# Kernel optimization log

Hardware: AMD Instinct MI355X
Metric: run time of the kernel (lower is better)

The kernel has to match this reference:

```python
import jax, jax.numpy as jnp
import numpy as np


def setup_inputs() -> dict:
    key = jax.random.key(0)
    k1, k2, k3 = jax.random.split(key, 3)
    B, L, C, H, W = 64, 64, 256, 8, 8
    z = jax.random.normal(k1, (B, L, C, H, W), dtype=jnp.float32)
    # KalmanFilter learned params: gain projection and state-transition (1x1 channel maps)
    W_gain = jax.random.normal(k2, (C, C), dtype=jnp.float32) * (1.0 / np.sqrt(C))
    b_gain = jnp.zeros((C,), dtype=jnp.float32)
    W_pred = jax.random.normal(k3, (C, C), dtype=jnp.float32) * (1.0 / np.sqrt(C))
    b_pred = jnp.zeros((C,), dtype=jnp.float32)
    return {"z": z, "W_gain": W_gain, "b_gain": b_gain, "W_pred": W_pred, "b_pred": b_pred}


def reference(z, W_gain, b_gain, W_pred, b_pred):
    # z: [B, L, C, H, W]
    # calc_gain: per-timestep 1x1 channel projection + sigmoid -> gain in (0,1)
    gain = jax.nn.sigmoid(
        jnp.einsum('oc,blchw->blohw', W_gain, z) + b_gain[:, None, None]
    )  # [B, L, C, H, W]

    def step(prev_z, inputs):
        z_i, k_i = inputs  # each [B, C, H, W]
        # predict on detached previous state (matches previous_z.detach())
        pz = jax.lax.stop_gradient(prev_z)
        z_prime = jnp.einsum('oc,bchw->bohw', W_pred, pz) + b_pred[:, None, None]
        # Kalman update: z_hat = z' + K * (z - z')
        z_hat = z_prime + k_i * (z_i - z_prime)
        return z_hat, None

    init = z[:, 0]  # step 0: z_hat = z[:, 0]
    z_seq = jnp.swapaxes(z[:, 1:], 0, 1)      # [L-1, B, C, H, W]
    k_seq = jnp.swapaxes(gain[:, 1:], 0, 1)   # [L-1, B, C, H, W]
    final, _ = jax.lax.scan(step, init, (z_seq, k_seq))
    return final  # [B, C, H, W]
```

## Files before the change

kernel.cpp:

```cpp
#include <hip/hip_runtime.h>

using f32x4  = __attribute__((ext_vector_type(4))) float;
using u16x8  = __attribute__((ext_vector_type(8))) unsigned short;
using u16x4  = __attribute__((ext_vector_type(4))) unsigned short;
using bf16x8 = __attribute__((ext_vector_type(8))) __bf16;

__device__ __forceinline__ unsigned short f2bf(float f){
  return __builtin_bit_cast(unsigned short, (__bf16)f);
}
__device__ __forceinline__ float bf2f(unsigned short h){
  return __builtin_bit_cast(float, ((unsigned int)h) << 16);
}
__device__ __forceinline__ unsigned short f2h(float f){
  return __builtin_bit_cast(unsigned short, (_Float16)f);
}
__device__ __forceinline__ float h2f(unsigned short h){
  return (float)__builtin_bit_cast(_Float16, h);
}
__device__ __forceinline__ f32x4 mfma_bf16(u16x8 a, u16x8 b, f32x4 c){
  return __builtin_amdgcn_mfma_f32_16x16x32_bf16(
      __builtin_bit_cast(bf16x8, a), __builtin_bit_cast(bf16x8, b), c, 0, 0, 0);
}
__device__ __forceinline__ float fast_sigmoid(float x){
  return __builtin_amdgcn_rcpf(1.0f + __builtin_amdgcn_exp2f(-1.44269504f * x));
}

constexpr int C_  = 256;
constexpr int L_  = 64;
constexpr int CHW = C_ * 64;


#define BAR_LDS() do {                                        \
    asm volatile("s_waitcnt lgkmcnt(0)" ::: "memory");        \
    __builtin_amdgcn_s_barrier();                             \
    asm volatile("" ::: "memory");                            \
  } while (0)


__global__ __launch_bounds__(512, 2)
void kalman_kernel(const float* __restrict__ z,  const float* __restrict__ Wg,
                   const float* __restrict__ bg, const float* __restrict__ Wp,
                   const float* __restrict__ bp, float* __restrict__ out)
{
  __shared__ unsigned short zbuf[4][4096];
  __shared__ unsigned short sbuf[2][4096];
  __shared__ unsigned short kbuf[2][4096];

  const int lx  = (int)blockIdx.x;
  const int xcd = lx & 7;
  const int loc = lx >> 3;
  const int b   = xcd + 8 * (loc >> 2);
  const int q   = loc & 3;

  const int t    = (int)threadIdx.x;
  const int lane = t & 63;
  const int wv   = t >> 6;
  const int role = wv >> 2;
  const int rw   = wv & 3;
  const int m    = lane & 15;
  const int g    = lane >> 4;

  const float* zg = z + (size_t)b * L_ * CHW + q * 16;

  const float* Wsel = (role == 0) ? Wp : Wg;
  const float* bsrc = (role == 0) ? bp : bg;
  u16x8 wf[4][8];
  f32x4 bsel[4];
  #pragma unroll
  for (int mi = 0; mi < 4; ++mi){
    const int mt = rw * 4 + mi;
    const float* src = Wsel + (size_t)(mt * 16 + m) * 256 + g * 8;
    #pragma unroll
    for (int kc = 0; kc < 8; ++kc){
      f32x4 a0 = *(const f32x4*)(src + kc * 32);
      f32x4 a1 = *(const f32x4*)(src + kc * 32 + 4);
      #pragma unroll
      for (int j = 0; j < 4; ++j){
        wf[mi][kc][j]     = f2bf(a0[j]);
        wf[mi][kc][j + 4] = f2bf(a1[j]);
      }
    }
    bsel[mi] = *(const f32x4*)(bsrc + mt * 16 + g * 4);
  }

  const int sp = t & 15;
  const int ss = t >> 4;
  const float* st_src = zg + ss * 8 * 64 + sp;
  const int st_dst = (ss * 16 + sp) * 8;
  const int boff   = g * 128 + m * 8;

  {
    float v0[8], v1[8], v2[8];
    #pragma unroll
    for (int j = 0; j < 8; ++j) v0[j] = st_src[j * 64];
    #pragma unroll
    for (int j = 0; j < 8; ++j) v1[j] = st_src[CHW + j * 64];
    #pragma unroll
    for (int j = 0; j < 8; ++j) v2[j] = st_src[2 * CHW + j * 64];
    u16x8 u0, u1, u2;
    #pragma unroll
    for (int j = 0; j < 8; ++j){ u0[j] = f2bf(v0[j]); u1[j] = f2bf(v1[j]); u2[j] = f2bf(v2[j]); }
    *(u16x8*)(&sbuf[0][st_dst]) = u0;
    *(u16x8*)(&zbuf[1][st_dst]) = u1;
    *(u16x8*)(&zbuf[2][st_dst]) = u2;
  }
  float pf[8];
  const float* pfp = st_src + 3 * (size_t)CHW;
  #pragma unroll
  for (int j = 0; j < 8; ++j) pf[j] = pfp[j * 64];
  pfp += CHW;
  __syncthreads();

  if (role == 1){
    u16x8 zf[8];
    #pragma unroll
    for (int kc = 0; kc < 8; ++kc) zf[kc] = *(const u16x8*)(&zbuf[1][kc * 512 + boff]);
    f32x4 gl[4] = {bsel[0], bsel[1], bsel[2], bsel[3]};
    #pragma unroll
    for (int kc = 0; kc < 8; ++kc)
      #pragma unroll
      for (int mi = 0; mi < 4; ++mi)
        gl[mi] = mfma_bf16(wf[mi][kc], zf[kc], gl[mi]);
    #pragma unroll
    for (int mi = 0; mi < 4; ++mi){
      const int ro = (rw * 4 + mi) * 16 + g * 4;
      const int el = ((ro >> 3) * 16 + m) * 8 + (ro & 7);
      u16x4 kk;
      #pragma unroll
      for (int r = 0; r < 4; ++r) kk[r] = f2h(fast_sigmoid(gl[mi][r]));
      *(u16x4*)(&kbuf[1][el]) = kk;
    }
  }
  __syncthreads();

  for (int l = 1; l < 63; ++l){
    if (role == 0){
      const unsigned short* sb  = sbuf[(l - 1) & 1];
      const unsigned short* zbl = zbuf[l & 3];
      const unsigned short* kb  = kbuf[l & 1];
      unsigned short* sbw = sbuf[l & 1];

      u16x8 sf[8];
      #pragma unroll
      for (int kc = 0; kc < 8; ++kc) sf[kc] = *(const u16x8*)(sb + kc * 512 + boff);
      u16x4 zi4[4], k4[4];
      #pragma unroll
      for (int mi = 0; mi < 4; ++mi){
        const int ro = (rw * 4 + mi) * 16 + g * 4;
        const int el = ((ro >> 3) * 16 + m) * 8 + (ro & 7);
        zi4[mi] = *(const u16x4*)(zbl + el);
        k4[mi]  = *(const u16x4*)(kb + el);
      }

      f32x4 zpA[4] = {bsel[0], bsel[1], bsel[2], bsel[3]};
      f32x4 zpB[4] = {{0,0,0,0},{0,0,0,0},{0,0,0,0},{0,0,0,0}};
      __builtin_amdgcn_s_setprio(1);
      #pragma unroll
      for (int kc = 0; kc < 4; ++kc)
        #pragma unroll
        for (int mi = 0; mi < 4; ++mi){
          zpA[mi] = mfma_bf16(wf[mi][kc],     sf[kc],     zpA[mi]);
          zpB[mi] = mfma_bf16(wf[mi][kc + 4], sf[kc + 4], zpB[mi]);
        }
      __builtin_amdgcn_s_setprio(0);

      #pragma unroll
      for (int mi = 0; mi < 4; ++mi){
        const int ro = (rw * 4 + mi) * 16 + g * 4;
        const int el = ((ro >> 3) * 16 + m) * 8 + (ro & 7);
        u16x4 sh;
        #pragma unroll
        for (int r = 0; r < 4; ++r){
          float zpr = zpA[mi][r] + zpB[mi][r];
          float zh  = zpr + h2f(k4[mi][r]) * (bf2f(zi4[mi][r]) - zpr);
          sh[r] = f2bf(zh);
        }
        *(u16x4*)(sbw + el) = sh;
      }

      if (l <= 61){
        u16x8 u;
        #pragma unroll
        for (int j = 0; j < 8; ++j) u[j] = f2bf(pf[j]);
        *(u16x8*)(&zbuf[(l + 2) & 3][st_dst]) = u;
      }
      if (l <= 60){
        #pragma unroll
        for (int j = 0; j < 8; ++j) pf[j] = pfp[j * 64];
        pfp += CHW;
      }
    } else {
      const unsigned short* zb = zbuf[(l + 1) & 3];
      unsigned short* kw = kbuf[(l + 1) & 1];

      u16x8 zf[8];
      #pragma unroll
      for (int kc = 0; kc < 8; ++kc) zf[kc] = *(const u16x8*)(zb + kc * 512 + boff);

      if (l <= 61){
        u16x8 u;
        #pragma unroll
        for (int j = 0; j < 8; ++j) u[j] = f2bf(pf[j]);
        *(u16x8*)(&zbuf[(l + 2) & 3][st_dst]) = u;
      }
      if (l <= 60){
        #pragma unroll
        for (int j = 0; j < 8; ++j) pf[j] = pfp[j * 64];
        pfp += CHW;
      }

      f32x4 gl[4] = {bsel[0], bsel[1], bsel[2], bsel[3]};
      #pragma unroll
      for (int kc = 0; kc < 8; ++kc)
        #pragma unroll
        for (int mi = 0; mi < 4; ++mi)
          gl[mi] = mfma_bf16(wf[mi][kc], zf[kc], gl[mi]);

      #pragma unroll
      for (int mi = 0; mi < 4; ++mi){
        const int ro = (rw * 4 + mi) * 16 + g * 4;
        const int el = ((ro >> 3) * 16 + m) * 8 + (ro & 7);
        u16x4 kk;
        #pragma unroll
        for (int r = 0; r < 4; ++r) kk[r] = f2h(fast_sigmoid(gl[mi][r]));
        *(u16x4*)(kw + el) = kk;
      }
    }

    BAR_LDS();
  }

  if (role == 0){
    const unsigned short* sb  = sbuf[0];
    const unsigned short* zbl = zbuf[3];
    const unsigned short* kb  = kbuf[1];

    u16x8 sf[8];
    #pragma unroll
    for (int kc = 0; kc < 8; ++kc) sf[kc] = *(const u16x8*)(sb + kc * 512 + boff);
    u16x4 zi4[4], k4[4];
    #pragma unroll
    for (int mi = 0; mi < 4; ++mi){
      const int ro = (rw * 4 + mi) * 16 + g * 4;
      const int el = ((ro >> 3) * 16 + m) * 8 + (ro & 7);
      zi4[mi] = *(const u16x4*)(zbl + el);
      k4[mi]  = *(const u16x4*)(kb + el);
    }

    f32x4 zpA[4] = {bsel[0], bsel[1], bsel[2], bsel[3]};
    f32x4 zpB[4] = {{0,0,0,0},{0,0,0,0},{0,0,0,0},{0,0,0,0}};
    #pragma unroll
    for (int kc = 0; kc < 4; ++kc)
      #pragma unroll
      for (int mi = 0; mi < 4; ++mi){
        zpA[mi] = mfma_bf16(wf[mi][kc],     sf[kc],     zpA[mi]);
        zpB[mi] = mfma_bf16(wf[mi][kc + 4], sf[kc + 4], zpB[mi]);
      }

    #pragma unroll
    for (int mi = 0; mi < 4; ++mi){
      const int ro = (rw * 4 + mi) * 16 + g * 4;
      float* o = out + ((size_t)b * 256 + ro) * 64 + q * 16 + m;
      #pragma unroll
      for (int r = 0; r < 4; ++r){
        float zpr = zpA[mi][r] + zpB[mi][r];
        o[r * 64] = zpr + h2f(k4[mi][r]) * (bf2f(zi4[mi][r]) - zpr);
      }
    }
  }
}

extern "C" void kernel_launch(void* const* d_in, const int* in_sizes, int n_in,
                              void* d_out, int out_size, void* d_ws, size_t ws_size,
                              hipStream_t stream)
{
  const float* z  = (const float*)d_in[0];
  const float* Wg = (const float*)d_in[1];
  const float* bg = (const float*)d_in[2];
  const float* Wp = (const float*)d_in[3];
  const float* bp = (const float*)d_in[4];
  float* out = (float*)d_out;
  hipLaunchKernelGGL(kalman_kernel, dim3(256), dim3(512), 0, stream,
                     z, Wg, bg, Wp, bp, out);
}
```

Baseline: 87.31 us.

## Halve block to 256 threads with each wave computing eight output tiles

Shrinks the workgroup from 8 waves to 4 (2 predict, 2 gain), so each wave now holds 8 row-tiles of weights in registers (64 u16x8 fragments) and issues twice as many MFMAs per step. Staging loads double per thread to cover the same tile. The dual-accumulator split for the predict chain is removed, giving a single chain of 8 dependent MFMAs per tile. The aim is to cut barrier cost per step and cross-wave overhead. The risks are heavy register pressure, possible spills, and a longer serial MFMA critical path on the sequential recurrence.

```diff
diff --git a/kernel.cpp b/kernel.cpp
--- a/kernel.cpp
+++ b/kernel.cpp
@@ -37,7 +37,7 @@
   } while (0)
 
 
-__global__ __launch_bounds__(512, 2)
+__global__ __launch_bounds__(256, 1)
 void kalman_kernel(const float* __restrict__ z,  const float* __restrict__ Wg,
                    const float* __restrict__ bg, const float* __restrict__ Wp,
                    const float* __restrict__ bp, float* __restrict__ out)
@@ -55,8 +55,8 @@
   const int t    = (int)threadIdx.x;
   const int lane = t & 63;
   const int wv   = t >> 6;
-  const int role = wv >> 2;
-  const int rw   = wv & 3;
+  const int role = wv >> 1;
+  const int rw   = wv & 1;
   const int m    = lane & 15;
   const int g    = lane >> 4;
 
@@ -64,11 +64,11 @@
 
   const float* Wsel = (role == 0) ? Wp : Wg;
   const float* bsrc = (role == 0) ? bp : bg;
-  u16x8 wf[4][8];
-  f32x4 bsel[4];
+  u16x8 wf[8][8];
+  f32x4 bsel[8];
   #pragma unroll
-  for (int mi = 0; mi < 4; ++mi){
-    const int mt = rw * 4 + mi;
+  for (int mi = 0; mi < 8; ++mi){
+    const int mt = rw * 8 + mi;
     const float* src = Wsel + (size_t)(mt * 16 + m) * 256 + g * 8;
     #pragma unroll
     for (int kc = 0; kc < 8; ++kc){
@@ -85,29 +85,39 @@
 
   const int sp = t & 15;
   const int ss = t >> 4;
-  const float* st_src = zg + ss * 8 * 64 + sp;
-  const int st_dst = (ss * 16 + sp) * 8;
-  const int boff   = g * 128 + m * 8;
+  const float* st_src = zg + ss * 16 * 64 + sp;
+  const int st_dst0 = ((ss * 2) * 16 + sp) * 8;
+  const int st_dst1 = ((ss * 2 + 1) * 16 + sp) * 8;
+  const int boff    = g * 128 + m * 8;
 
   {
-    float v0[8], v1[8], v2[8];
-    #pragma unroll
-    for (int j = 0; j < 8; ++j) v0[j] = st_src[j * 64];
-    #pragma unroll
-    for (int j = 0; j < 8; ++j) v1[j] = st_src[CHW + j * 64];
-    #pragma unroll
-    for (int j = 0; j < 8; ++j) v2[j] = st_src[2 * CHW + j * 64];
-    u16x8 u0, u1, u2;
-    #pragma unroll
-    for (int j = 0; j < 8; ++j){ u0[j] = f2bf(v0[j]); u1[j] = f2bf(v1[j]); u2[j] = f2bf(v2[j]); }
-    *(u16x8*)(&sbuf[0][st_dst]) = u0;
-    *(u16x8*)(&zbuf[1][st_dst]) = u1;
-    *(u16x8*)(&zbuf[2][st_dst]) = u2;
-  }
-  float pf[8];
+    u16x8 a0, a1;
+    #pragma unroll
+    for (int j = 0; j < 8; ++j){
+      a0[j] = f2bf(st_src[j * 64]);
+      a1[j] = f2bf(st_src[(j + 8) * 64]);
+    }
+    *(u16x8*)(&sbuf[0][st_dst0]) = a0;
+    *(u16x8*)(&sbuf[0][st_dst1]) = a1;
+    #pragma unroll
+    for (int j = 0; j < 8; ++j){
+      a0[j] = f2bf(st_src[CHW + j * 64]);
+      a1[j] = f2bf(st_src[CHW + (j + 8) * 64]);
+    }
+    *(u16x8*)(&zbuf[1][st_dst0]) = a0;
+    *(u16x8*)(&zbuf[1][st_dst1]) = a1;
+    #pragma unroll
+    for (int j = 0; j < 8; ++j){
+      a0[j] = f2bf(st_src[2 * CHW + j * 64]);
+      a1[j] = f2bf(st_src[2 * CHW + (j + 8) * 64]);
+    }
+    *(u16x8*)(&zbuf[2][st_dst0]) = a0;
+    *(u16x8*)(&zbuf[2][st_dst1]) = a1;
+  }
+  float pf[16];
   const float* pfp = st_src + 3 * (size_t)CHW;
   #pragma unroll
-  for (int j = 0; j < 8; ++j) pf[j] = pfp[j * 64];
+  for (int j = 0; j < 16; ++j) pf[j] = pfp[j * 64];
   pfp += CHW;
   __syncthreads();
 
@@ -115,15 +125,16 @@
     u16x8 zf[8];
     #pragma unroll
     for (int kc = 0; kc < 8; ++kc) zf[kc] = *(const u16x8*)(&zbuf[1][kc * 512 + boff]);
-    f32x4 gl[4] = {bsel[0], bsel[1], bsel[2], bsel[3]};
+    f32x4 gl[8] = {bsel[0], bsel[1], bsel[2], bsel[3],
+                   bsel[4], bsel[5], bsel[6], bsel[7]};
     #pragma unroll
     for (int kc = 0; kc < 8; ++kc)
       #pragma unroll
-      for (int mi = 0; mi < 4; ++mi)
+      for (int mi = 0; mi < 8; ++mi)
         gl[mi] = mfma_bf16(wf[mi][kc], zf[kc], gl[mi]);
     #pragma unroll
-    for (int mi = 0; mi < 4; ++mi){
-      const int ro = (rw * 4 + mi) * 16 + g * 4;
+    for (int mi = 0; mi < 8; ++mi){
+      const int ro = (rw * 8 + mi) * 16 + g * 4;
       const int el = ((ro >> 3) * 16 + m) * 8 + (ro & 7);
       u16x4 kk;
       #pragma unroll
@@ -143,35 +154,33 @@
       u16x8 sf[8];
       #pragma unroll
       for (int kc = 0; kc < 8; ++kc) sf[kc] = *(const u16x8*)(sb + kc * 512 + boff);
-      u16x4 zi4[4], k4[4];
-      #pragma unroll
-      for (int mi = 0; mi < 4; ++mi){
-        const int ro = (rw * 4 + mi) * 16 + g * 4;
+      u16x4 zi4[8], k4[8];
+      #pragma unroll
+      for (int mi = 0; mi < 8; ++mi){
+        const int ro = (rw * 8 + mi) * 16 + g * 4;
         const int el = ((ro >> 3) * 16 + m) * 8 + (ro & 7);
         zi4[mi] = *(const u16x4*)(zbl + el);
         k4[mi]  = *(const u16x4*)(kb + el);
       }
 
-      f32x4 zpA[4] = {bsel[0], bsel[1], bsel[2], bsel[3]};
-      f32x4 zpB[4] = {{0,0,0,0},{0,0,0,0},{0,0,0,0},{0,0,0,0}};
+      f32x4 zp[8] = {bsel[0], bsel[1], bsel[2], bsel[3],
+                     bsel[4], bsel[5], bsel[6], bsel[7]};
       __builtin_amdgcn_s_setprio(1);
       #pragma unroll
-      for (int kc = 0; kc < 4; ++kc)
-        #pragma unroll
-        for (int mi = 0; mi < 4; ++mi){
-          zpA[mi] = mfma_bf16(wf[mi][kc],     sf[kc],     zpA[mi]);
-          zpB[mi] = mfma_bf16(wf[mi][kc + 4], sf[kc + 4], zpB[mi]);
-        }
+      for (int kc = 0; kc < 8; ++kc)
+        #pragma unroll
+        for (int mi = 0; mi < 8; ++mi)
+          zp[mi] = mfma_bf16(wf[mi][kc], sf[kc], zp[mi]);
       __builtin_amdgcn_s_setprio(0);
 
       #pragma unroll
-      for (int mi = 0; mi < 4; ++mi){
-        const int ro = (rw * 4 + mi) * 16 + g * 4;
+      for (int mi = 0; mi < 8; ++mi){
+        const int ro = (rw * 8 + mi) * 16 + g * 4;
         const int el = ((ro >> 3) * 16 + m) * 8 + (ro & 7);
         u16x4 sh;
         #pragma unroll
         for (int r = 0; r < 4; ++r){
-          float zpr = zpA[mi][r] + zpB[mi][r];
+          float zpr = zp[mi][r];
           float zh  = zpr + h2f(k4[mi][r]) * (bf2f(zi4[mi][r]) - zpr);
           sh[r] = f2bf(zh);
         }
@@ -179,14 +188,15 @@
       }
 
       if (l <= 61){
-        u16x8 u;
-        #pragma unroll
-        for (int j = 0; j < 8; ++j) u[j] = f2bf(pf[j]);
-        *(u16x8*)(&zbuf[(l + 2) & 3][st_dst]) = u;
+        u16x8 a0, a1;
+        #pragma unroll
+        for (int j = 0; j < 8; ++j){ a0[j] = f2bf(pf[j]); a1[j] = f2bf(pf[j + 8]); }
+        *(u16x8*)(&zbuf[(l + 2) & 3][st_dst0]) = a0;
+        *(u16x8*)(&zbuf[(l + 2) & 3][st_dst1]) = a1;
       }
       if (l <= 60){
         #pragma unroll
-        for (int j = 0; j < 8; ++j) pf[j] = pfp[j * 64];
+        for (int j = 0; j < 16; ++j) pf[j] = pfp[j * 64];
         pfp += CHW;
       }
     } else {
@@ -198,27 +208,29 @@
       for (int kc = 0; kc < 8; ++kc) zf[kc] = *(const u16x8*)(zb + kc * 512 + boff);
 
       if (l <= 61){
-        u16x8 u;
-        #pragma unroll
-        for (int j = 0; j < 8; ++j) u[j] = f2bf(pf[j]);
-        *(u16x8*)(&zbuf[(l + 2) & 3][st_dst]) = u;
+        u16x8 a0, a1;
+        #pragma unroll
+        for (int j = 0; j < 8; ++j){ a0[j] = f2bf(pf[j]); a1[j] = f2bf(pf[j + 8]); }
+        *(u16x8*)(&zbuf[(l + 2) & 3][st_dst0]) = a0;
+        *(u16x8*)(&zbuf[(l + 2) & 3][st_dst1]) = a1;
       }
       if (l <= 60){
         #pragma unroll
-        for (int j = 0; j < 8; ++j) pf[j] = pfp[j * 64];
+        for (int j = 0; j < 16; ++j) pf[j] = pfp[j * 64];
         pfp += CHW;
       }
 
-      f32x4 gl[4] = {bsel[0], bsel[1], bsel[2], bsel[3]};
+      f32x4 gl[8] = {bsel[0], bsel[1], bsel[2], bsel[3],
+                     bsel[4], bsel[5], bsel[6], bsel[7]};
       #pragma unroll
       for (int kc = 0; kc < 8; ++kc)
         #pragma unroll
-        for (int mi = 0; mi < 4; ++mi)
+        for (int mi = 0; mi < 8; ++mi)
           gl[mi] = mfma_bf16(wf[mi][kc], zf[kc], gl[mi]);
 
       #pragma unroll
-      for (int mi = 0; mi < 4; ++mi){
-        const int ro = (rw * 4 + mi) * 16 + g * 4;
+      for (int mi = 0; mi < 8; ++mi){
+        const int ro = (rw * 8 + mi) * 16 + g * 4;
         const int el = ((ro >> 3) * 16 + m) * 8 + (ro & 7);
         u16x4 kk;
         #pragma unroll
@@ -238,32 +250,30 @@
     u16x8 sf[8];
     #pragma unroll
     for (int kc = 0; kc < 8; ++kc) sf[kc] = *(const u16x8*)(sb + kc * 512 + boff);
-    u16x4 zi4[4], k4[4];
-    #pragma unroll
-    for (int mi = 0; mi < 4; ++mi){
-      const int ro = (rw * 4 + mi) * 16 + g * 4;
+    u16x4 zi4[8], k4[8];
+    #pragma unroll
+    for (int mi = 0; mi < 8; ++mi){
+      const int ro = (rw * 8 + mi) * 16 + g * 4;
       const int el = ((ro >> 3) * 16 + m) * 8 + (ro & 7);
       zi4[mi] = *(const u16x4*)(zbl + el);
       k4[mi]  = *(const u16x4*)(kb + el);
     }
 
-    f32x4 zpA[4] = {bsel[0], bsel[1], bsel[2], bsel[3]};
-    f32x4 zpB[4] = {{0,0,0,0},{0,0,0,0},{0,0,0,0},{0,0,0,0}};
-    #pragma unroll
-    for (int kc = 0; kc < 4; ++kc)
-      #pragma unroll
-      for (int mi = 0; mi < 4; ++mi){
-        zpA[mi] = mfma_bf16(wf[mi][kc],     sf[kc],     zpA[mi]);
-        zpB[mi] = mfma_bf16(wf[mi][kc + 4], sf[kc + 4], zpB[mi]);
-      }
-
-    #pragma unroll
-    for (int mi = 0; mi < 4; ++mi){
-      const int ro = (rw * 4 + mi) * 16 + g * 4;
+    f32x4 zp[8] = {bsel[0], bsel[1], bsel[2], bsel[3],
+                   bsel[4], bsel[5], bsel[6], bsel[7]};
+    #pragma unroll
+    for (int kc = 0; kc < 8; ++kc)
+      #pragma unroll
+      for (int mi = 0; mi < 8; ++mi)
+        zp[mi] = mfma_bf16(wf[mi][kc], sf[kc], zp[mi]);
+
+    #pragma unroll
+    for (int mi = 0; mi < 8; ++mi){
+      const int ro = (rw * 8 + mi) * 16 + g * 4;
       float* o = out + ((size_t)b * 256 + ro) * 64 + q * 16 + m;
       #pragma unroll
       for (int r = 0; r < 4; ++r){
-        float zpr = zpA[mi][r] + zpB[mi][r];
+        float zpr = zp[mi][r];
         o[r * 64] = zpr + h2f(k4[mi][r]) * (bf2f(zi4[mi][r]) - zpr);
       }
     }
@@ -280,6 +290,6 @@
   const float* Wp = (const float*)d_in[3];
   const float* bp = (const float*)d_in[4];
   float* out = (float*)d_out;
-  hipLaunchKernelGGL(kalman_kernel, dim3(256), dim3(512), 0, stream,
+  hipLaunchKernelGGL(kalman_kernel, dim3(256), dim3(256), 0, stream,
                      z, Wg, bg, Wp, bp, out);
 }
```

Measured after the change: 130.5 us. 49.5% more time.
